# Kernel tuning notes

Measured on AMD Instinct MI355X. Metric: run time of the kernel, lower is better.

Reference implementation:

```python
import jax, jax.numpy as jnp
import numpy as np

N_NODES = 100000
N_EDGES = 3200000
D = 64


def setup_inputs() -> dict:
    key = jax.random.key(0)
    ks = jax.random.split(key, 8)
    x = jax.random.normal(ks[0], (N_NODES, D), dtype=jnp.float32)
    adj_row = jnp.sort(jax.random.randint(ks[1], (N_EDGES,), 0, N_NODES, dtype=jnp.int32)).astype(jnp.int64)
    adj_col = jax.random.randint(ks[2], (N_EDGES,), 0, N_NODES, dtype=jnp.int32).astype(jnp.int64)
    adj_val = jax.random.uniform(ks[3], (N_EDGES,), dtype=jnp.float32)
    stdv = 1.0 / np.sqrt(D)
    W1 = jax.random.uniform(ks[4], (D, D), minval=-stdv, maxval=stdv, dtype=jnp.float32)
    b1 = jax.random.uniform(ks[5], (D,), minval=-stdv, maxval=stdv, dtype=jnp.float32)
    W2 = jax.random.uniform(ks[6], (D, D), minval=-stdv, maxval=stdv, dtype=jnp.float32)
    b2 = jax.random.uniform(ks[7], (D,), minval=-stdv, maxval=stdv, dtype=jnp.float32)
    return {"x": x, "adj_row": adj_row, "adj_col": adj_col, "adj_val": adj_val,
            "W1": W1, "b1": b1, "W2": W2, "b2": b2}


def _spmm(row, col, val, support):
    # output[i] = sum_{e: row[e]==i} val[e] * support[col[e]]  (COO SpMM)
    return jax.ops.segment_sum(val[:, None] * support[col], row, num_segments=N_NODES)


def _gc_layer(x, row, col, val, W, b):
    support = x @ W            # dense mm [N, D]
    out = _spmm(row, col, val, support)
    return out + b


def reference(x, adj_row, adj_col, adj_val, W1, b1, W2, b2):
    # layer 0 + LeakyReLU(0.2)
    h = _gc_layer(x, adj_row, adj_col, adj_val, W1, b1)
    h = jnp.where(h >= 0, h, 0.2 * h)
    # dropout is identity in eval mode
    # layer 1 (no activation)
    out = _gc_layer(h, adj_row, adj_col, adj_val, W2, b2)
    return out
```

## Files before the change

### kernel.cpp

```cpp
#include <hip/hip_runtime.h>

#define NN 100000
#define NE 3200000
#define DD 64
#define KE 64
#define NW (NE / KE)
#define GEMM_BLOCKS 391
#define PREP_BLOCKS 12501

typedef unsigned int uint32;

__device__ inline uint32 bf16_rne(float f) {
    uint32 u = __float_as_uint(f);
    return (u + 0x7fffu + ((u >> 16) & 1u)) >> 16;
}

__device__ inline void quant_store(const float* acc, uint32* __restrict__ qrow,
                                   float* __restrict__ scp) {
    float m = 0.f;
#pragma unroll
    for (int j = 0; j < DD; ++j) m = fmaxf(m, fabsf(acc[j]));
    float inv = (m > 0.f) ? (127.f / m) : 0.f;
    *scp = m * (1.f / 127.f);
#pragma unroll
    for (int q = 0; q < 16; ++q) {
        uint32 p = 0;
#pragma unroll
        for (int b = 0; b < 4; ++b) {
            int v = (int)rintf(acc[4 * q + b] * inv) + 128;
            p |= ((uint32)v) << (8 * b);
        }
        qrow[q] = p;
    }
}

__global__ __launch_bounds__(256) void pre_kernel(
    const void* rowbuf, const void* colbuf, const float* __restrict__ val,
    const float* __restrict__ x, const float* __restrict__ W1,
    uint32* __restrict__ erec, int* __restrict__ rp, int* __restrict__ ws,
    uint32* __restrict__ qt, float* __restrict__ sc) {
    __shared__ float4 sW[DD * 16];

    if (blockIdx.x < GEMM_BLOCKS) {
        for (int i = threadIdx.x; i < DD * 16; i += 256)
            sW[i] = ((const float4*)W1)[i];
        __syncthreads();

        int row = blockIdx.x * 256 + threadIdx.x;
        if (row >= NN) return;

        float acc[DD];
#pragma unroll
        for (int j = 0; j < DD; ++j) acc[j] = 0.f;

        const float4* Bp = (const float4*)(x + (size_t)row * DD);
#pragma unroll
        for (int k4 = 0; k4 < 16; ++k4) {
            float4 x4 = Bp[k4];
            float xs[4] = {x4.x, x4.y, x4.z, x4.w};
#pragma unroll
            for (int kk = 0; kk < 4; ++kk) {
                float xk = xs[kk];
                int k = 4 * k4 + kk;
#pragma unroll
                for (int j4 = 0; j4 < 16; ++j4) {
                    float4 w = sW[k * 16 + j4];
                    acc[4 * j4 + 0] = fmaf(xk, w.x, acc[4 * j4 + 0]);
                    acc[4 * j4 + 1] = fmaf(xk, w.y, acc[4 * j4 + 1]);
                    acc[4 * j4 + 2] = fmaf(xk, w.z, acc[4 * j4 + 2]);
                    acc[4 * j4 + 3] = fmaf(xk, w.w, acc[4 * j4 + 3]);
                }
            }
        }
        quant_store(acc, qt + (size_t)row * 16, sc + row);
        return;
    }

    int e = (blockIdx.x - GEMM_BLOCKS) * 256 + threadIdx.x;
    if (e >= NE + 32) return;
    if (e >= NE) { erec[e] = 0u; return; }

    const int* p32 = (const int*)rowbuf;
    bool is64 = (p32[NE / 2 + 1] == 0 && p32[NE / 2] != 0);

    int r, rn, c;
    if (is64) {
        const long long* row = (const long long*)rowbuf;
        const long long* col = (const long long*)colbuf;
        r  = (int)row[e];
        rn = (e == NE - 1) ? NN : (int)row[e + 1];
        c  = (int)col[e];
    } else {
        const int* row = (const int*)rowbuf;
        const int* col = (const int*)colbuf;
        r  = row[e];
        rn = (e == NE - 1) ? NN : row[e + 1];
        c  = col[e];
    }
    erec[e] = ((bf16_rne(val[e]) & 0x7fffu) << 17) | (uint32)c;
    for (int q = r + 1; q <= rn; ++q) rp[q] = e + 1;
    if (e == 0) {
        for (int q = 0; q <= r; ++q) rp[q] = 0;
        ws[0]  = 0;
        ws[NW] = NN;
    }
    if (((e + 1) & (KE - 1)) == 0 && (e + 1) < NE)
        ws[(e + 1) / KE] = r + 1;
}

#define ISSUE(G, S, V, I) {                                     \
    uint32 t_ = (uint32)__shfl((int)rw, (I), 16);               \
    uint32 c_ = t_ & 0x1ffffu;                                  \
    G = qt[((size_t)c_ << 4) + (uint32)sl];                     \
    S = sc[c_];                                                 \
    V = __uint_as_float((t_ >> 17) << 16); }

#define FLUSH() {                                                       \
    float cr_ = fmaf(-128.f, ts, 0.f);                                  \
    float y0 = a0 + cr_ + bv.x, y1 = a1 + cr_ + bv.y,                   \
          y2 = a2 + cr_ + bv.z, y3 = a3 + cr_ + bv.w;                   \
    if (L1) {                                                           \
        y0 = (y0 >= 0.f) ? y0 : 0.2f * y0;                              \
        y1 = (y1 >= 0.f) ? y1 : 0.2f * y1;                              \
        y2 = (y2 >= 0.f) ? y2 : 0.2f * y2;                              \
        y3 = (y3 >= 0.f) ? y3 : 0.2f * y3;                              \
        unsigned long long pk =                                         \
            (unsigned long long)(bf16_rne(y0) | (bf16_rne(y1) << 16)) | \
            ((unsigned long long)(bf16_rne(y2) | (bf16_rne(y3) << 16)) << 32); \
        __builtin_nontemporal_store(pk,                                 \
            (unsigned long long*)((uint2*)obv + (size_t)rr * 16 + sl)); \
    } else {                                                            \
        float* op = (float*)obv + (size_t)rr * 64 + sl * 4;             \
        __builtin_nontemporal_store(y0, op);                            \
        __builtin_nontemporal_store(y1, op + 1);                        \
        __builtin_nontemporal_store(y2, op + 2);                        \
        __builtin_nontemporal_store(y3, op + 3);                        \
    }                                                                   \
    a0 = 0.f; a1 = 0.f; a2 = 0.f; a3 = 0.f; ts = 0.f; ++rr; }

#define ACCUM(G, S, V, I) {                                     \
    while (e0 + (I) >= re) {                                    \
        FLUSH();                                                \
        re = (rr < r1) ? rp[rr + 1] : 0x7fffffff;               \
    }                                                           \
    float t_ = V * S;                                           \
    a0 = fmaf(t_, (float)(G & 0xffu),         a0);              \
    a1 = fmaf(t_, (float)((G >> 8) & 0xffu),  a1);              \
    a2 = fmaf(t_, (float)((G >> 16) & 0xffu), a2);              \
    a3 = fmaf(t_, (float)(G >> 24),           a3);              \
    ts += t_; }

template <bool L1>
__global__ __launch_bounds__(256) void spmm_kernel(
    const uint32* __restrict__ qt, const float* __restrict__ sc,
    const uint32* __restrict__ erec, const int* __restrict__ rp,
    const int* __restrict__ ws, const float* __restrict__ bias,
    void* __restrict__ obv) {
    int worker = (blockIdx.x * blockDim.x + threadIdx.x) >> 4;
    int sl = threadIdx.x & 15;
    if (worker >= NW) return;

    int rr = ws[worker];
    int r1 = ws[worker + 1];
    if (rr >= r1) return;

    const float4 bv = ((const float4*)bias)[sl];

    int eb = rp[rr];
    int ee = rp[r1];
    int re = rp[rr + 1];
    float a0 = 0.f, a1 = 0.f, a2 = 0.f, a3 = 0.f, ts = 0.f;

    for (int e0 = eb; e0 < ee; e0 += 16) {
        uint32 rw = __builtin_nontemporal_load(&erec[e0 + sl]);
        rw = (e0 + sl < ee) ? rw : 0u;
        uint32 g0, g1, g2, g3, g4, g5, g6, g7;
        float  s0, s1, s2, s3, s4, s5, s6, s7;
        float  v0, v1, v2, v3, v4, v5, v6, v7;
        ISSUE(g0, s0, v0, 0)  ISSUE(g1, s1, v1, 1)
        ISSUE(g2, s2, v2, 2)  ISSUE(g3, s3, v3, 3)
        ISSUE(g4, s4, v4, 4)  ISSUE(g5, s5, v5, 5)
        ISSUE(g6, s6, v6, 6)  ISSUE(g7, s7, v7, 7)
        ACCUM(g0, s0, v0, 0)  ACCUM(g1, s1, v1, 1)
        ACCUM(g2, s2, v2, 2)  ACCUM(g3, s3, v3, 3)
        ACCUM(g4, s4, v4, 4)  ACCUM(g5, s5, v5, 5)
        ACCUM(g6, s6, v6, 6)  ACCUM(g7, s7, v7, 7)
        ISSUE(g0, s0, v0, 8)  ISSUE(g1, s1, v1, 9)
        ISSUE(g2, s2, v2, 10) ISSUE(g3, s3, v3, 11)
        ISSUE(g4, s4, v4, 12) ISSUE(g5, s5, v5, 13)
        ISSUE(g6, s6, v6, 14) ISSUE(g7, s7, v7, 15)
        ACCUM(g0, s0, v0, 8)  ACCUM(g1, s1, v1, 9)
        ACCUM(g2, s2, v2, 10) ACCUM(g3, s3, v3, 11)
        ACCUM(g4, s4, v4, 12) ACCUM(g5, s5, v5, 13)
        ACCUM(g6, s6, v6, 14) ACCUM(g7, s7, v7, 15)
    }
    while (rr < r1) { FLUSH(); }
}

__global__ __launch_bounds__(256) void gemm_bb_kernel(
    const uint32* __restrict__ Bb, const float* __restrict__ W,
    uint32* __restrict__ qt, float* __restrict__ sc) {
    __shared__ float4 sW[DD * 16];
    for (int i = threadIdx.x; i < DD * 16; i += 256)
        sW[i] = ((const float4*)W)[i];
    __syncthreads();

    int row = blockIdx.x * 256 + threadIdx.x;
    if (row >= NN) return;

    float acc[DD];
#pragma unroll
    for (int j = 0; j < DD; ++j) acc[j] = 0.f;

    const uint4* Bp = (const uint4*)(Bb + (size_t)row * 32);
#pragma unroll
    for (int q4 = 0; q4 < 8; ++q4) {
        uint4 u4 = Bp[q4];
        uint32 us[4] = {u4.x, u4.y, u4.z, u4.w};
#pragma unroll
        for (int t = 0; t < 4; ++t) {
            int k = q4 * 8 + t * 2;
            float x0 = __uint_as_float(us[t] << 16);
            float x1 = __uint_as_float(us[t] & 0xffff0000u);
#pragma unroll
            for (int j4 = 0; j4 < 16; ++j4) {
                float4 w0 = sW[k * 16 + j4];
                float4 w1 = sW[(k + 1) * 16 + j4];
                acc[4 * j4 + 0] = fmaf(x0, w0.x, acc[4 * j4 + 0]);
                acc[4 * j4 + 1] = fmaf(x0, w0.y, acc[4 * j4 + 1]);
                acc[4 * j4 + 2] = fmaf(x0, w0.z, acc[4 * j4 + 2]);
                acc[4 * j4 + 3] = fmaf(x0, w0.w, acc[4 * j4 + 3]);
                acc[4 * j4 + 0] = fmaf(x1, w1.x, acc[4 * j4 + 0]);
                acc[4 * j4 + 1] = fmaf(x1, w1.y, acc[4 * j4 + 1]);
                acc[4 * j4 + 2] = fmaf(x1, w1.z, acc[4 * j4 + 2]);
                acc[4 * j4 + 3] = fmaf(x1, w1.w, acc[4 * j4 + 3]);
            }
        }
    }
    quant_store(acc, qt + (size_t)row * 16, sc + row);
}

extern "C" void kernel_launch(void* const* d_in, const int* in_sizes, int n_in,
                              void* d_out, int out_size, void* d_ws, size_t ws_size,
                              hipStream_t stream) {
    const float* x       = (const float*)d_in[0];
    const void*  adj_row = d_in[1];
    const void*  adj_col = d_in[2];
    const float* adj_val = (const float*)d_in[3];
    const float* W1      = (const float*)d_in[4];
    const float* b1      = (const float*)d_in[5];
    const float* W2      = (const float*)d_in[6];
    const float* b2      = (const float*)d_in[7];
    float*       out     = (float*)d_out;

    uint32* bufA = (uint32*)d_ws;
    uint32* qt   = bufA + (size_t)NN * 32;
    float*  sc   = (float*)(qt + (size_t)NN * 16);
    uint32* erec = (uint32*)(sc + NN);
    int*    rp   = (int*)(erec + NE + 32);
    int*    wst  = rp + (NN + 1);

    const int spmm_blocks = (NW * 16) / 256;

    pre_kernel<<<GEMM_BLOCKS + PREP_BLOCKS, 256, 0, stream>>>(
        adj_row, adj_col, adj_val, x, W1, erec, rp, wst, qt, sc);

    spmm_kernel<true><<<spmm_blocks, 256, 0, stream>>>(qt, sc, erec, rp, wst,
                                                       b1, bufA);

    gemm_bb_kernel<<<GEMM_BLOCKS, 256, 0, stream>>>(bufA, W2, qt, sc);

    spmm_kernel<false><<<spmm_blocks, 256, 0, stream>>>(qt, sc, erec, rp, wst,
                                                        b2, out);
}
```

Measured before the change: 185.6 us.

## Use signed int8 quantization and issue all 16 gathers before accumulating

Switches the quantized support rows from offset-128 unsigned bytes to signed int8. This removes the per-edge running scale sum and the correction term applied at flush. The SpMM loop now issues all 16 row gathers before any accumulation and prefetches the next edge-record chunk, which raises memory-level parallelism at the cost of more live registers. It also replaces the nontemporal loads and stores with plain vector loads and stores. The prefetch reads up to 16 entries past the edge range, which the existing 32-entry padding in the edge buffer covers.

New measurement: 185.8 us. About the same (+0.1%).

```diff
diff --git a/kernel.cpp b/kernel.cpp
--- a/kernel.cpp
+++ b/kernel.cpp
@@ -15,8 +15,9 @@
     return (u + 0x7fffu + ((u >> 16) & 1u)) >> 16;
 }
 
-__device__ inline void quant_store(const float* acc, uint32* __restrict__ qrow,
-                                   float* __restrict__ scp) {
+__device__ inline void quant_store_s8(const float* acc,
+                                      uint32* __restrict__ qrow,
+                                      float* __restrict__ scp) {
     float m = 0.f;
 #pragma unroll
     for (int j = 0; j < DD; ++j) m = fmaxf(m, fabsf(acc[j]));
@@ -27,8 +28,8 @@
         uint32 p = 0;
 #pragma unroll
         for (int b = 0; b < 4; ++b) {
-            int v = (int)rintf(acc[4 * q + b] * inv) + 128;
-            p |= ((uint32)v) << (8 * b);
+            int v = (int)rintf(acc[4 * q + b] * inv);
+            p |= ((uint32)(v & 0xff)) << (8 * b);
         }
         qrow[q] = p;
     }
@@ -72,7 +73,7 @@
                 }
             }
         }
-        quant_store(acc, qt + (size_t)row * 16, sc + row);
+        quant_store_s8(acc, qt + (size_t)row * 16, sc + row);
         return;
     }
 
@@ -108,47 +109,41 @@
         ws[(e + 1) / KE] = r + 1;
 }
 
-#define ISSUE(G, S, V, I) {                                     \
-    uint32 t_ = (uint32)__shfl((int)rw, (I), 16);               \
-    uint32 c_ = t_ & 0x1ffffu;                                  \
+#define ISSUE(G, S, I) {                                        \
+    uint32 u_ = (uint32)__shfl((int)rwm, (I), 16);              \
+    uint32 c_ = u_ & 0x1ffffu;                                  \
     G = qt[((size_t)c_ << 4) + (uint32)sl];                     \
-    S = sc[c_];                                                 \
-    V = __uint_as_float((t_ >> 17) << 16); }
+    S = sc[c_]; }
 
 #define FLUSH() {                                                       \
-    float cr_ = fmaf(-128.f, ts, 0.f);                                  \
-    float y0 = a0 + cr_ + bv.x, y1 = a1 + cr_ + bv.y,                   \
-          y2 = a2 + cr_ + bv.z, y3 = a3 + cr_ + bv.w;                   \
+    float y0 = a0 + bv.x, y1 = a1 + bv.y,                               \
+          y2 = a2 + bv.z, y3 = a3 + bv.w;                               \
     if (L1) {                                                           \
         y0 = (y0 >= 0.f) ? y0 : 0.2f * y0;                              \
         y1 = (y1 >= 0.f) ? y1 : 0.2f * y1;                              \
         y2 = (y2 >= 0.f) ? y2 : 0.2f * y2;                              \
         y3 = (y3 >= 0.f) ? y3 : 0.2f * y3;                              \
-        unsigned long long pk =                                         \
-            (unsigned long long)(bf16_rne(y0) | (bf16_rne(y1) << 16)) | \
-            ((unsigned long long)(bf16_rne(y2) | (bf16_rne(y3) << 16)) << 32); \
-        __builtin_nontemporal_store(pk,                                 \
-            (unsigned long long*)((uint2*)obv + (size_t)rr * 16 + sl)); \
+        uint2 pk_;                                                      \
+        pk_.x = bf16_rne(y0) | (bf16_rne(y1) << 16);                    \
+        pk_.y = bf16_rne(y2) | (bf16_rne(y3) << 16);                    \
+        ((uint2*)obv)[(size_t)rr * 16 + sl] = pk_;                      \
     } else {                                                            \
-        float* op = (float*)obv + (size_t)rr * 64 + sl * 4;             \
-        __builtin_nontemporal_store(y0, op);                            \
-        __builtin_nontemporal_store(y1, op + 1);                        \
-        __builtin_nontemporal_store(y2, op + 2);                        \
-        __builtin_nontemporal_store(y3, op + 3);                        \
+        float4 f4_ = make_float4(y0, y1, y2, y3);                       \
+        ((float4*)obv)[(size_t)rr * 16 + sl] = f4_;                     \
     }                                                                   \
-    a0 = 0.f; a1 = 0.f; a2 = 0.f; a3 = 0.f; ts = 0.f; ++rr; }
-
-#define ACCUM(G, S, V, I) {                                     \
+    a0 = 0.f; a1 = 0.f; a2 = 0.f; a3 = 0.f; ++rr; }
+
+#define ACCUM(G, S, I) {                                        \
     while (e0 + (I) >= re) {                                    \
         FLUSH();                                                \
         re = (rr < r1) ? rp[rr + 1] : 0x7fffffff;               \
     }                                                           \
-    float t_ = V * S;                                           \
-    a0 = fmaf(t_, (float)(G & 0xffu),         a0);              \
-    a1 = fmaf(t_, (float)((G >> 8) & 0xffu),  a1);              \
-    a2 = fmaf(t_, (float)((G >> 16) & 0xffu), a2);              \
-    a3 = fmaf(t_, (float)(G >> 24),           a3);              \
-    ts += t_; }
+    uint32 u_ = (uint32)__shfl((int)rwm, (I), 16);              \
+    float t_ = __uint_as_float((u_ >> 17) << 16) * S;           \
+    a0 = fmaf(t_, (float)((int)(G << 24) >> 24), a0);           \
+    a1 = fmaf(t_, (float)((int)(G << 16) >> 24), a1);           \
+    a2 = fmaf(t_, (float)((int)(G <<  8) >> 24), a2);           \
+    a3 = fmaf(t_, (float)((int)G         >> 24), a3); }
 
 template <bool L1>
 __global__ __launch_bounds__(256) void spmm_kernel(
@@ -169,30 +164,24 @@
     int eb = rp[rr];
     int ee = rp[r1];
     int re = rp[rr + 1];
-    float a0 = 0.f, a1 = 0.f, a2 = 0.f, a3 = 0.f, ts = 0.f;
-
+    float a0 = 0.f, a1 = 0.f, a2 = 0.f, a3 = 0.f;
+
+    uint32 rwc = erec[eb + sl];
     for (int e0 = eb; e0 < ee; e0 += 16) {
-        uint32 rw = __builtin_nontemporal_load(&erec[e0 + sl]);
-        rw = (e0 + sl < ee) ? rw : 0u;
+        uint32 rwm = (e0 + sl < ee) ? rwc : 0u;
         uint32 g0, g1, g2, g3, g4, g5, g6, g7;
+        uint32 h0, h1, h2, h3, h4, h5, h6, h7;
         float  s0, s1, s2, s3, s4, s5, s6, s7;
-        float  v0, v1, v2, v3, v4, v5, v6, v7;
-        ISSUE(g0, s0, v0, 0)  ISSUE(g1, s1, v1, 1)
-        ISSUE(g2, s2, v2, 2)  ISSUE(g3, s3, v3, 3)
-        ISSUE(g4, s4, v4, 4)  ISSUE(g5, s5, v5, 5)
-        ISSUE(g6, s6, v6, 6)  ISSUE(g7, s7, v7, 7)
-        ACCUM(g0, s0, v0, 0)  ACCUM(g1, s1, v1, 1)
-        ACCUM(g2, s2, v2, 2)  ACCUM(g3, s3, v3, 3)
-        ACCUM(g4, s4, v4, 4)  ACCUM(g5, s5, v5, 5)
-        ACCUM(g6, s6, v6, 6)  ACCUM(g7, s7, v7, 7)
-        ISSUE(g0, s0, v0, 8)  ISSUE(g1, s1, v1, 9)
-        ISSUE(g2, s2, v2, 10) ISSUE(g3, s3, v3, 11)
-        ISSUE(g4, s4, v4, 12) ISSUE(g5, s5, v5, 13)
-        ISSUE(g6, s6, v6, 14) ISSUE(g7, s7, v7, 15)
-        ACCUM(g0, s0, v0, 8)  ACCUM(g1, s1, v1, 9)
-        ACCUM(g2, s2, v2, 10) ACCUM(g3, s3, v3, 11)
-        ACCUM(g4, s4, v4, 12) ACCUM(g5, s5, v5, 13)
-        ACCUM(g6, s6, v6, 14) ACCUM(g7, s7, v7, 15)
+        float  t0, t1, t2, t3, t4, t5, t6, t7;
+        ISSUE(g0, s0, 0)  ISSUE(g1, s1, 1)  ISSUE(g2, s2, 2)  ISSUE(g3, s3, 3)
+        ISSUE(g4, s4, 4)  ISSUE(g5, s5, 5)  ISSUE(g6, s6, 6)  ISSUE(g7, s7, 7)
+        ISSUE(h0, t0, 8)  ISSUE(h1, t1, 9)  ISSUE(h2, t2, 10) ISSUE(h3, t3, 11)
+        ISSUE(h4, t4, 12) ISSUE(h5, t5, 13) ISSUE(h6, t6, 14) ISSUE(h7, t7, 15)
+        rwc = erec[e0 + 16 + sl];
+        ACCUM(g0, s0, 0)  ACCUM(g1, s1, 1)  ACCUM(g2, s2, 2)  ACCUM(g3, s3, 3)
+        ACCUM(g4, s4, 4)  ACCUM(g5, s5, 5)  ACCUM(g6, s6, 6)  ACCUM(g7, s7, 7)
+        ACCUM(h0, t0, 8)  ACCUM(h1, t1, 9)  ACCUM(h2, t2, 10) ACCUM(h3, t3, 11)
+        ACCUM(h4, t4, 12) ACCUM(h5, t5, 13) ACCUM(h6, t6, 14) ACCUM(h7, t7, 15)
     }
     while (rr < r1) { FLUSH(); }
 }
@@ -237,7 +226,7 @@
             }
         }
     }
-    quant_store(acc, qt + (size_t)row * 16, sc + row);
+    quant_store_s8(acc, qt + (size_t)row * 16, sc + row);
 }
 
 extern "C" void kernel_launch(void* const* d_in, const int* in_sizes, int n_in,
```
